# Optimization experiments

Hardware: AMD Instinct MI355X
Metric: run time of the kernel (lower is better)

Reference implementation:

```python
import jax, jax.numpy as jnp
import numpy as np

ALPHA, GAMMA = 0.25, 2.0
THR = 0.85            # soft_target_threshold
KL_EPS = 1e-6
FOCAL_EPS = 1e-8
VOC = 96              # len(vocab); index VOC is blank/pad


def setup_inputs() -> dict:
    key = jax.random.key(0)
    ks = jax.random.split(key, 6)
    bs, nq, n_pts, num_gt, L = 16, 200, 25, 32, 25
    return {
        "pred_logits": jax.random.normal(ks[0], (bs, nq, n_pts, 1), jnp.float32),
        "pred_ctrl_points": jax.random.uniform(ks[1], (bs, nq, n_pts, 2), jnp.float32),
        "pred_text_logits": jax.random.normal(ks[2], (bs, nq, n_pts, VOC + 1), jnp.float32),
        "tgt_ctrl_points": jax.random.uniform(ks[3], (bs, num_gt, n_pts, 2), jnp.float32),
        "tgt_texts": jax.random.randint(ks[4], (bs, num_gt, L), 0, VOC + 1),
        "centroids": jax.random.normal(ks[5], (VOC, 256), jnp.float32),
    }


def _cost_matrix(pred_logits, pred_ctrl_points, pred_text_logits,
                 tgt_ctrl_points, tgt_texts, centroids):
    bs, nq, n_pts, _ = pred_logits.shape
    num_gt = tgt_texts.shape[1]

    # ---- focal classification cost (mean over control points) ----
    out_prob = jax.nn.sigmoid(pred_logits.reshape(bs * nq, n_pts, -1))
    neg = (1.0 - ALPHA) * out_prob ** GAMMA * (-jnp.log1p(-(out_prob - FOCAL_EPS)))
    neg = (1.0 - ALPHA) * out_prob ** GAMMA * (-jnp.log(1.0 - out_prob + FOCAL_EPS))
    pos = ALPHA * (1.0 - out_prob) ** GAMMA * (-jnp.log(out_prob + FOCAL_EPS))
    cost_class = (pos[..., 0] - neg[..., 0]).mean(-1, keepdims=True)  # [bs*nq, 1]

    # ---- L1 cdist over flattened control points ----
    out_pts = pred_ctrl_points.reshape(bs * nq, n_pts * 2)
    tgt_pts = tgt_ctrl_points.reshape(bs * num_gt, n_pts * 2)
    cost_kpts = jnp.abs(out_pts[:, None, :] - tgt_pts[None, :, :]).sum(-1)  # [bs*nq, bs*num_gt]

    # ---- linguistic KL-div cost (per-batch block diagonal) ----
    probs = jax.nn.softmax(pred_text_logits, axis=-1)          # [bs,nq,n_pts,VOC+1]
    pred_avg = probs[..., :VOC].mean(axis=2)                   # [bs,nq,VOC]
    P = pred_avg + KL_EPS
    P = P / P.sum(-1, keepdims=True)
    logP = jnp.log(P)

    # soft target distribution per character (generate_soft_target_sequence)
    cn = centroids / jnp.linalg.norm(centroids, axis=-1, keepdims=True)
    soft_all = THR * jnp.eye(VOC, dtype=P.dtype) + (1.0 - THR) * jax.nn.softmax(cn @ cn.T, axis=-1)  # [VOC,VOC]

    mask = (tgt_texts != VOC)                                  # [bs,num_gt,L]
    lengths = mask.sum(-1)                                     # [bs,num_gt]
    per_char = soft_all[jnp.clip(tgt_texts, 0, VOC - 1)]       # [bs,num_gt,L,VOC]
    tgt_avg = (per_char * mask[..., None]).sum(2) / jnp.maximum(lengths, 1)[..., None].astype(P.dtype)
    T = tgt_avg + KL_EPS
    T = T / T.sum(-1, keepdims=True)                           # [bs,num_gt,VOC]

    # KL(T || P) = sum T*logT - sum T*logP, vectorized over (query, gt)
    kl = (T * jnp.log(T)).sum(-1)[:, None, :] - jnp.einsum('bqv,bgv->bqg', logP, T)  # [bs,nq,num_gt]
    kl = jnp.where(lengths[:, None, :] == 0, 100.0, kl)

    # place per-batch blocks on the diagonal of the global cost matrix
    eye = jnp.eye(bs, dtype=kl.dtype)
    cost_text = jnp.einsum('bqg,bc->bqcg', kl, eye).reshape(bs * nq, bs * num_gt)

    C = 1.0 * cost_class + 1.0 * cost_kpts + 1.0 * cost_text   # class/coord/text weights = 1
    return C.reshape(bs, nq, bs * num_gt)


def reference(pred_logits, pred_ctrl_points, pred_text_logits,
              tgt_ctrl_points, tgt_texts, centroids):
    return _cost_matrix(pred_logits, pred_ctrl_points, pred_text_logits,
                        tgt_ctrl_points, tgt_texts, centroids)
```

## Files before the change

kernel.cpp:

```cpp
#include <hip/hip_runtime.h>
#include <hip/hip_bf16.h>

#define BS 16
#define NQ 200
#define NPTS 25
#define VOC 96
#define VOCP1 97
#define NGT 32
#define LSEQ 25
#define NCOL (BS*NGT)
#define NBQ (BS*NQ)
#define KL_EPS 1e-6f
#define FOCAL_EPS 1e-8f

__global__ __launch_bounds__(128) void kA(
        const float* __restrict__ pred_logits,
        const float* __restrict__ pred_text_logits,
        const float* __restrict__ centroids,
        float* __restrict__ logP,
        float* __restrict__ cost_class,
        float* __restrict__ soft)
{
    const int tid  = threadIdx.x;
    const int wave = tid >> 6, lane = tid & 63;
    __shared__ float s_buf[NPTS * VOCP1];
    __shared__ float s_invden[NPTS];
    __shared__ float s_part[2];

    if (blockIdx.x < NBQ) {
        const int bq = blockIdx.x;
        const float* tl = pred_text_logits + (size_t)bq * NPTS * VOCP1;
        for (int i = tid; i < NPTS * VOCP1; i += 128)
            s_buf[i] = __expf(tl[i]);
        __syncthreads();

        const int grp = tid >> 5, sub = tid & 31;
        for (int p0 = 0; p0 < NPTS; p0 += 4) {
            int p = p0 + grp;
            float s = 0.f;
            if (p < NPTS)
                for (int v = sub; v < VOCP1; v += 32) s += s_buf[p * VOCP1 + v];
            #pragma unroll
            for (int off = 16; off; off >>= 1) s += __shfl_xor(s, off, 32);
            if (p < NPTS && sub == 0) s_invden[p] = 1.0f / s;
        }

        if (wave == 0) {
            float cc = 0.f;
            if (lane < NPTS) {
                float x = pred_logits[bq * NPTS + lane];
                float p = 1.f / (1.f + __expf(-x));
                float pos = 0.25f * (1.f - p) * (1.f - p) * (-__logf(p + FOCAL_EPS));
                float neg = 0.75f * p * p * (-__logf(1.f - p + FOCAL_EPS));
                cc = pos - neg;
            }
            #pragma unroll
            for (int off = 32; off; off >>= 1) cc += __shfl_xor(cc, off);
            if (lane == 0) cost_class[bq] = cc * (1.0f / NPTS);
        }
        __syncthreads();

        float avg = 0.f;
        if (tid < VOC) {
            float a = 0.f;
            #pragma unroll
            for (int p = 0; p < NPTS; p++)
                a += s_buf[p * VOCP1 + tid] * s_invden[p];
            avg = a * (1.0f / NPTS);
        }
        float s = avg;
        #pragma unroll
        for (int off = 32; off; off >>= 1) s += __shfl_xor(s, off);
        if (lane == 0) s_part[wave] = s;
        __syncthreads();
        float denom = s_part[0] + s_part[1] + (float)VOC * KL_EPS;
        if (tid < VOC)
            logP[(size_t)bq * VOC + tid] = __logf((avg + KL_EPS) / denom);
    } else {
        const int i = blockIdx.x - NBQ;
        for (int k = tid; k < 64; k += 128)
            *(float4*)&s_buf[k * 4] = *(const float4*)&centroids[i * 256 + k * 4];
        __syncthreads();

        float e = 0.f;
        if (tid < VOC) {
            float dij = 0.f, djj = 0.f, dii = 0.f;
            const float4* cj = (const float4*)(centroids + (size_t)tid * 256);
            #pragma unroll 4
            for (int k = 0; k < 64; k++) {
                float4 b = cj[k];
                float4 a = *(const float4*)&s_buf[k * 4];
                dij += a.x * b.x + a.y * b.y + a.z * b.z + a.w * b.w;
                djj += b.x * b.x + b.y * b.y + b.z * b.z + b.w * b.w;
                dii += a.x * a.x + a.y * a.y + a.z * a.z + a.w * a.w;
            }
            float sim = dij * rsqrtf(dii * djj);
            e = __expf(sim);
        }
        float s = e;
        #pragma unroll
        for (int off = 32; off; off >>= 1) s += __shfl_xor(s, off);
        if (lane == 0) s_part[wave] = s;
        __syncthreads();
        float den = s_part[0] + s_part[1];
        if (tid < VOC) {
            float v = 0.15f * e / den;
            if (tid == i) v += 0.85f;
            soft[i * VOC + tid] = v;
        }
    }
}

__global__ __launch_bounds__(256) void kC(
        const float* __restrict__ pred_ctrl,
        const float* __restrict__ tgt_ctrl,
        const float* __restrict__ logP,
        const float* __restrict__ cost_class,
        const float* __restrict__ soft,
        const int* __restrict__ tgt_texts,
        float* __restrict__ out)
{
    const int rt   = blockIdx.x >> 1;
    const int ch   = blockIdx.x & 1;
    const int row0 = rt * NPTS;
    const int c0   = ch * 256;
    const int b    = rt >> 3;
    const int tid  = threadIdx.x;

    __shared__ float s_pred[NPTS][52];
    __shared__ float s_logP[NPTS][VOC];
    __shared__ float s_T[NGT][VOCP1];
    __shared__ float s_text[NPTS][NGT + 1];
    __shared__ float s_cc[NPTS];
    __shared__ int   s_chars[NGT][LSEQ];
    __shared__ float s_TlogT[NGT];
    __shared__ int   s_len[NGT];

    const bool has_text = ((b < 8) == (ch == 0));
    const int  jb0 = b * NGT - c0;

    const float* pg = pred_ctrl + (size_t)row0 * 50;
    for (int i = tid; i < NPTS * 50; i += 256) {
        int r = i / 50;
        s_pred[r][i - r * 50] = pg[i];
    }
    if (tid < NPTS) s_cc[tid] = cost_class[row0 + tid];
    if (has_text) {
        for (int i = tid; i < NPTS * VOC; i += 256) {
            int r = i / VOC, v = i - r * VOC;
            s_logP[r][v] = logP[(size_t)(row0 + r) * VOC + v];
        }
        for (int i = tid; i < NGT * LSEQ; i += 256) {
            int g = i / LSEQ, l = i - g * LSEQ;
            s_chars[g][l] = tgt_texts[(b * NGT + g) * LSEQ + l];
        }
    }

    float tg[50];
    {
        const float2* trow = (const float2*)(tgt_ctrl + (size_t)(c0 + tid) * 50);
        #pragma unroll
        for (int q = 0; q < 25; q++) {
            float2 v = trow[q];
            tg[2 * q] = v.x; tg[2 * q + 1] = v.y;
        }
    }
    __syncthreads();

    if (has_text) {
        const int grp = tid >> 5, sub = tid & 31;
        for (int g = grp; g < NGT; g += 8) {
            int len = 0;
            float a0 = 0.f, a1 = 0.f, a2 = 0.f;
            for (int l = 0; l < LSEQ; l++) {
                int t = s_chars[g][l];
                if (t != VOC) {
                    len++;
                    const float* sr = soft + t * VOC;
                    a0 += sr[sub]; a1 += sr[sub + 32]; a2 += sr[sub + 64];
                }
            }
            float inv = 1.f / (float)(len > 0 ? len : 1);
            a0 *= inv; a1 *= inv; a2 *= inv;
            float s = a0 + a1 + a2;
            #pragma unroll
            for (int off = 16; off; off >>= 1) s += __shfl_xor(s, off, 32);
            float denom = s + (float)VOC * KL_EPS;
            float t0 = (a0 + KL_EPS) / denom;
            float t1 = (a1 + KL_EPS) / denom;
            float t2 = (a2 + KL_EPS) / denom;
            s_T[g][sub] = t0; s_T[g][sub + 32] = t1; s_T[g][sub + 64] = t2;
            float tl = t0 * __logf(t0) + t1 * __logf(t1) + t2 * __logf(t2);
            #pragma unroll
            for (int off = 16; off; off >>= 1) tl += __shfl_xor(tl, off, 32);
            if (sub == 0) { s_TlogT[g] = tl; s_len[g] = len; }
        }
        __syncthreads();

        for (int i = tid; i < NPTS * NGT; i += 256) {
            int r = i >> 5, g = i & 31;
            float txt;
            if (s_len[g] == 0) {
                txt = 100.f;
            } else {
                float d0 = 0.f, d1 = 0.f;
                #pragma unroll
                for (int v = 0; v < VOC; v += 2) {
                    d0 += s_logP[r][v]     * s_T[g][v];
                    d1 += s_logP[r][v + 1] * s_T[g][v + 1];
                }
                txt = s_TlogT[g] - (d0 + d1);
            }
            s_text[r][g] = txt;
        }
        __syncthreads();
    }

    for (int r = 0; r < NPTS; r++) {
        float kp0 = 0.f, kp1 = 0.f, kp2 = 0.f, kp3 = 0.f;
        #pragma unroll
        for (int q = 0; q < 12; q++) {
            float4 p = *(const float4*)&s_pred[r][q * 4];
            kp0 += fabsf(p.x - tg[q * 4 + 0]);
            kp1 += fabsf(p.y - tg[q * 4 + 1]);
            kp2 += fabsf(p.z - tg[q * 4 + 2]);
            kp3 += fabsf(p.w - tg[q * 4 + 3]);
        }
        kp0 += fabsf(s_pred[r][48] - tg[48]);
        kp1 += fabsf(s_pred[r][49] - tg[49]);
        float val = s_cc[r] + (kp0 + kp1) + (kp2 + kp3);
        if (has_text) {
            unsigned g = (unsigned)((int)tid - jb0);
            if (g < (unsigned)NGT) val += s_text[r][g];
        }
        out[(size_t)(row0 + r) * NCOL + (c0 + tid)] = val;
    }
}

extern "C" void kernel_launch(void* const* d_in, const int* in_sizes, int n_in,
                              void* d_out, int out_size, void* d_ws, size_t ws_size,
                              hipStream_t stream) {
    const float* pred_logits = (const float*)d_in[0];
    const float* pred_ctrl   = (const float*)d_in[1];
    const float* pred_text   = (const float*)d_in[2];
    const float* tgt_ctrl    = (const float*)d_in[3];
    const int*   tgt_texts   = (const int*)d_in[4];
    const float* centroids   = (const float*)d_in[5];
    float* out = (float*)d_out;

    float* ws        = (float*)d_ws;
    float* logP      = ws;
    float* costclass = logP + (size_t)NBQ * VOC;
    float* soft      = costclass + NBQ;

    kA<<<NBQ + VOC, 128, 0, stream>>>(pred_logits, pred_text, centroids,
                                      logP, costclass, soft);
    kC<<<256, 256, 0, stream>>>(pred_ctrl, tgt_ctrl, logP, costclass,
                                soft, tgt_texts, out);
}
```

Measured before the change: 132.3 us.

## Split cost kernel into target-dist, register-tiled L1 cdist, and text-KL add kernels

Splits the combined kernel into three. kB computes the per-target soft distributions T once per batch, where each kC block used to recompute them. kC computes the L1 cdist as a 64x64 register-blocked tile with 4x4 outputs per thread. kT adds the block-diagonal KL term into the output with a read-modify-write. The aim is to remove redundant T computation and improve reuse and occupancy in the cdist. The cost is two extra launches and a second pass over part of the output.

```diff
diff --git a/kernel.cpp b/kernel.cpp
--- a/kernel.cpp
+++ b/kernel.cpp
@@ -111,130 +111,161 @@
     }
 }
 
+__global__ __launch_bounds__(256) void kB(
+        const int* __restrict__ tgt_texts,
+        const float* __restrict__ soft,
+        float* __restrict__ T,
+        float* __restrict__ TlogT,
+        int* __restrict__ lens)
+{
+    const int b   = blockIdx.x;
+    const int tid = threadIdx.x;
+    __shared__ float s_soft[VOC * VOC];
+    __shared__ int   s_chars[NGT][LSEQ];
+
+    for (int i = tid; i < VOC * VOC / 4; i += 256)
+        ((float4*)s_soft)[i] = ((const float4*)soft)[i];
+    for (int i = tid; i < NGT * LSEQ; i += 256)
+        s_chars[i / LSEQ][i % LSEQ] = tgt_texts[b * NGT * LSEQ + i];
+    __syncthreads();
+
+    const int grp = tid >> 5, sub = tid & 31;
+    for (int g = grp; g < NGT; g += 8) {
+        int len = 0;
+        float a0 = 0.f, a1 = 0.f, a2 = 0.f;
+        for (int l = 0; l < LSEQ; l++) {
+            int t = s_chars[g][l];
+            if (t != VOC) {
+                len++;
+                const float* sr = s_soft + t * VOC;
+                a0 += sr[sub]; a1 += sr[sub + 32]; a2 += sr[sub + 64];
+            }
+        }
+        float inv = 1.f / (float)(len > 0 ? len : 1);
+        a0 *= inv; a1 *= inv; a2 *= inv;
+        float s = a0 + a1 + a2;
+        #pragma unroll
+        for (int off = 16; off; off >>= 1) s += __shfl_xor(s, off, 32);
+        float denom = s + (float)VOC * KL_EPS;
+        float t0 = (a0 + KL_EPS) / denom;
+        float t1 = (a1 + KL_EPS) / denom;
+        float t2 = (a2 + KL_EPS) / denom;
+        const int bg = b * NGT + g;
+        T[(size_t)bg * VOC + sub]      = t0;
+        T[(size_t)bg * VOC + sub + 32] = t1;
+        T[(size_t)bg * VOC + sub + 64] = t2;
+        float tl = t0 * __logf(t0) + t1 * __logf(t1) + t2 * __logf(t2);
+        #pragma unroll
+        for (int off = 16; off; off >>= 1) tl += __shfl_xor(tl, off, 32);
+        if (sub == 0) { TlogT[bg] = tl; lens[bg] = len; }
+    }
+}
+
+#define TR 64
+#define TC 64
 __global__ __launch_bounds__(256) void kC(
         const float* __restrict__ pred_ctrl,
         const float* __restrict__ tgt_ctrl,
+        const float* __restrict__ cost_class,
+        float* __restrict__ out)
+{
+    const int r0  = (blockIdx.x >> 3) * TR;
+    const int c0  = (blockIdx.x & 7) * TC;
+    const int tid = threadIdx.x;
+    const int tx  = tid & 15;
+    const int ty  = tid >> 4;
+
+    __shared__ float s_p[TR][52];
+    __shared__ float s_t[TC][52];
+    __shared__ float s_cc[TR];
+
+    const float* pg = pred_ctrl + (size_t)r0 * 50;
+    const float* tg = tgt_ctrl + (size_t)c0 * 50;
+    for (int i = tid; i < TR * 50; i += 256) {
+        int r = i / 50, d = i - r * 50;
+        s_p[r][d] = pg[i];
+        s_t[r][d] = tg[i];
+    }
+    if (tid < TR) s_cc[tid] = cost_class[r0 + tid];
+    __syncthreads();
+
+    float acc[4][4];
+    #pragma unroll
+    for (int i = 0; i < 4; i++)
+        #pragma unroll
+        for (int j = 0; j < 4; j++) acc[i][j] = 0.f;
+
+    #pragma unroll
+    for (int k = 0; k < 48; k += 4) {
+        float4 p[4], t[4];
+        #pragma unroll
+        for (int i = 0; i < 4; i++) p[i] = *(const float4*)&s_p[ty * 4 + i][k];
+        #pragma unroll
+        for (int j = 0; j < 4; j++) t[j] = *(const float4*)&s_t[tx + 16 * j][k];
+        #pragma unroll
+        for (int i = 0; i < 4; i++)
+            #pragma unroll
+            for (int j = 0; j < 4; j++)
+                acc[i][j] += fabsf(p[i].x - t[j].x) + fabsf(p[i].y - t[j].y)
+                           + fabsf(p[i].z - t[j].z) + fabsf(p[i].w - t[j].w);
+    }
+    {
+        float2 p[4], t[4];
+        #pragma unroll
+        for (int i = 0; i < 4; i++) p[i] = *(const float2*)&s_p[ty * 4 + i][48];
+        #pragma unroll
+        for (int j = 0; j < 4; j++) t[j] = *(const float2*)&s_t[tx + 16 * j][48];
+        #pragma unroll
+        for (int i = 0; i < 4; i++)
+            #pragma unroll
+            for (int j = 0; j < 4; j++)
+                acc[i][j] += fabsf(p[i].x - t[j].x) + fabsf(p[i].y - t[j].y);
+    }
+
+    #pragma unroll
+    for (int i = 0; i < 4; i++) {
+        const int row = ty * 4 + i;
+        const float cc = s_cc[row];
+        #pragma unroll
+        for (int j = 0; j < 4; j++)
+            out[(size_t)(r0 + row) * NCOL + c0 + tx + 16 * j] = acc[i][j] + cc;
+    }
+}
+
+__global__ __launch_bounds__(256) void kT(
         const float* __restrict__ logP,
-        const float* __restrict__ cost_class,
-        const float* __restrict__ soft,
-        const int* __restrict__ tgt_texts,
+        const float* __restrict__ T,
+        const float* __restrict__ TlogT,
+        const int* __restrict__ lens,
         float* __restrict__ out)
 {
-    const int rt   = blockIdx.x >> 1;
-    const int ch   = blockIdx.x & 1;
-    const int row0 = rt * NPTS;
-    const int c0   = ch * 256;
-    const int b    = rt >> 3;
-    const int tid  = threadIdx.x;
-
-    __shared__ float s_pred[NPTS][52];
-    __shared__ float s_logP[NPTS][VOC];
-    __shared__ float s_T[NGT][VOCP1];
-    __shared__ float s_text[NPTS][NGT + 1];
-    __shared__ float s_cc[NPTS];
-    __shared__ int   s_chars[NGT][LSEQ];
-    __shared__ float s_TlogT[NGT];
+    const int r0  = blockIdx.x * 8;
+    const int b   = r0 / NQ;
+    const int tid = threadIdx.x;
+    __shared__ float s_lp[8][VOC];
+    __shared__ float s_Tt[VOC][NGT + 1];
+    __shared__ float s_tl[NGT];
     __shared__ int   s_len[NGT];
 
-    const bool has_text = ((b < 8) == (ch == 0));
-    const int  jb0 = b * NGT - c0;
-
-    const float* pg = pred_ctrl + (size_t)row0 * 50;
-    for (int i = tid; i < NPTS * 50; i += 256) {
-        int r = i / 50;
-        s_pred[r][i - r * 50] = pg[i];
-    }
-    if (tid < NPTS) s_cc[tid] = cost_class[row0 + tid];
-    if (has_text) {
-        for (int i = tid; i < NPTS * VOC; i += 256) {
-            int r = i / VOC, v = i - r * VOC;
-            s_logP[r][v] = logP[(size_t)(row0 + r) * VOC + v];
-        }
-        for (int i = tid; i < NGT * LSEQ; i += 256) {
-            int g = i / LSEQ, l = i - g * LSEQ;
-            s_chars[g][l] = tgt_texts[(b * NGT + g) * LSEQ + l];
-        }
-    }
-
-    float tg[50];
-    {
-        const float2* trow = (const float2*)(tgt_ctrl + (size_t)(c0 + tid) * 50);
-        #pragma unroll
-        for (int q = 0; q < 25; q++) {
-            float2 v = trow[q];
-            tg[2 * q] = v.x; tg[2 * q + 1] = v.y;
-        }
+    for (int i = tid; i < 8 * VOC; i += 256)
+        s_lp[i / VOC][i % VOC] = logP[(size_t)r0 * VOC + i];
+    for (int i = tid; i < NGT * VOC; i += 256) {
+        int g = i / VOC, v = i - g * VOC;
+        s_Tt[v][g] = T[(size_t)(b * NGT) * VOC + i];
+    }
+    if (tid < NGT) {
+        s_tl[tid]  = TlogT[b * NGT + tid];
+        s_len[tid] = lens[b * NGT + tid];
     }
     __syncthreads();
 
-    if (has_text) {
-        const int grp = tid >> 5, sub = tid & 31;
-        for (int g = grp; g < NGT; g += 8) {
-            int len = 0;
-            float a0 = 0.f, a1 = 0.f, a2 = 0.f;
-            for (int l = 0; l < LSEQ; l++) {
-                int t = s_chars[g][l];
-                if (t != VOC) {
-                    len++;
-                    const float* sr = soft + t * VOC;
-                    a0 += sr[sub]; a1 += sr[sub + 32]; a2 += sr[sub + 64];
-                }
-            }
-            float inv = 1.f / (float)(len > 0 ? len : 1);
-            a0 *= inv; a1 *= inv; a2 *= inv;
-            float s = a0 + a1 + a2;
-            #pragma unroll
-            for (int off = 16; off; off >>= 1) s += __shfl_xor(s, off, 32);
-            float denom = s + (float)VOC * KL_EPS;
-            float t0 = (a0 + KL_EPS) / denom;
-            float t1 = (a1 + KL_EPS) / denom;
-            float t2 = (a2 + KL_EPS) / denom;
-            s_T[g][sub] = t0; s_T[g][sub + 32] = t1; s_T[g][sub + 64] = t2;
-            float tl = t0 * __logf(t0) + t1 * __logf(t1) + t2 * __logf(t2);
-            #pragma unroll
-            for (int off = 16; off; off >>= 1) tl += __shfl_xor(tl, off, 32);
-            if (sub == 0) { s_TlogT[g] = tl; s_len[g] = len; }
-        }
-        __syncthreads();
-
-        for (int i = tid; i < NPTS * NGT; i += 256) {
-            int r = i >> 5, g = i & 31;
-            float txt;
-            if (s_len[g] == 0) {
-                txt = 100.f;
-            } else {
-                float d0 = 0.f, d1 = 0.f;
-                #pragma unroll
-                for (int v = 0; v < VOC; v += 2) {
-                    d0 += s_logP[r][v]     * s_T[g][v];
-                    d1 += s_logP[r][v + 1] * s_T[g][v + 1];
-                }
-                txt = s_TlogT[g] - (d0 + d1);
-            }
-            s_text[r][g] = txt;
-        }
-        __syncthreads();
-    }
-
-    for (int r = 0; r < NPTS; r++) {
-        float kp0 = 0.f, kp1 = 0.f, kp2 = 0.f, kp3 = 0.f;
-        #pragma unroll
-        for (int q = 0; q < 12; q++) {
-            float4 p = *(const float4*)&s_pred[r][q * 4];
-            kp0 += fabsf(p.x - tg[q * 4 + 0]);
-            kp1 += fabsf(p.y - tg[q * 4 + 1]);
-            kp2 += fabsf(p.z - tg[q * 4 + 2]);
-            kp3 += fabsf(p.w - tg[q * 4 + 3]);
-        }
-        kp0 += fabsf(s_pred[r][48] - tg[48]);
-        kp1 += fabsf(s_pred[r][49] - tg[49]);
-        float val = s_cc[r] + (kp0 + kp1) + (kp2 + kp3);
-        if (has_text) {
-            unsigned g = (unsigned)((int)tid - jb0);
-            if (g < (unsigned)NGT) val += s_text[r][g];
-        }
-        out[(size_t)(row0 + r) * NCOL + (c0 + tid)] = val;
-    }
+    const int g = tid & 31, rs = tid >> 5;
+    float d = 0.f;
+    #pragma unroll 8
+    for (int v = 0; v < VOC; v++) d += s_lp[rs][v] * s_Tt[v][g];
+    float val = (s_len[g] == 0) ? 100.f : (s_tl[g] - d);
+    size_t o = (size_t)(r0 + rs) * NCOL + b * NGT + g;
+    out[o] += val;
 }
 
 extern "C" void kernel_launch(void* const* d_in, const int* in_sizes, int n_in,
@@ -252,9 +283,13 @@
     float* logP      = ws;
     float* costclass = logP + (size_t)NBQ * VOC;
     float* soft      = costclass + NBQ;
+    float* T         = soft + VOC * VOC;
+    float* TlogT     = T + (size_t)NCOL * VOC;
+    int*   lens      = (int*)(TlogT + NCOL);
 
     kA<<<NBQ + VOC, 128, 0, stream>>>(pred_logits, pred_text, centroids,
                                       logP, costclass, soft);
-    kC<<<256, 256, 0, stream>>>(pred_ctrl, tgt_ctrl, logP, costclass,
-                                soft, tgt_texts, out);
-}
+    kB<<<BS, 256, 0, stream>>>(tgt_texts, soft, T, TlogT, lens);
+    kC<<<400, 256, 0, stream>>>(pred_ctrl, tgt_ctrl, costclass, out);
+    kT<<<400, 256, 0, stream>>>(logP, T, TlogT, lens, out);
+}
```

After: 127.3 us. -3.7%, faster.
